# Kernel optimization log

Measured on AMD Instinct MI355X. Metric: run time of the kernel, lower is better.

Reference implementation:

```python
import jax, jax.numpy as jnp
import numpy as np
import math

N_HEAD = 32
HEAD_DIM = 64
ROTARY_DIM = 32
ROTARY_BASE = 10000.0
NEG_INF = -10000.0


def _rope_cos_sin(seqlen):
    # RotaryEmbedding._update_cos_sin_cache: inv_freq over even indices of rotary_dim
    inv_freq = 1.0 / (ROTARY_BASE ** (jnp.arange(0, ROTARY_DIM, 2, dtype=jnp.float32) / ROTARY_DIM))
    t = jnp.arange(seqlen, dtype=jnp.float32)
    freqs = jnp.outer(t, inv_freq)  # [s, rd/2]
    return jnp.cos(freqs), jnp.sin(freqs)


def _apply_rotary(t, cos, sin):
    # t: [b, s, h, d]; GPT-NeoX half-rotation on first ROTARY_DIM dims, pass-through rest
    half = ROTARY_DIM // 2
    x1 = t[..., :half]
    x2 = t[..., half:ROTARY_DIM]
    x_pass = t[..., ROTARY_DIM:]
    c = cos[:, None, :]  # [s, 1, rd/2] -> broadcasts over (b, s, h, rd/2)
    s_ = sin[:, None, :]
    return jnp.concatenate([x1 * c - x2 * s_, x1 * s_ + x2 * c, x_pass], axis=-1)


def setup_inputs() -> dict:
    key = jax.random.key(0)
    k1, k2, k3, k4, k5 = jax.random.split(key, 5)
    b, s, e = 2, 2048, 2048
    return {
        "x": jax.random.normal(k1, (b, s, e), dtype=jnp.float32),
        "Wqkv": jax.random.normal(k2, (e, 3 * e), dtype=jnp.float32) * 0.02,
        "bqkv": jax.random.normal(k3, (3 * e,), dtype=jnp.float32) * 0.02,
        "Wout": jax.random.normal(k4, (e, e), dtype=jnp.float32) * 0.02,
        "bout": jax.random.normal(k5, (e,), dtype=jnp.float32) * 0.02,
    }


def reference(x, Wqkv, bqkv, Wout, bout):
    b, s, e = x.shape
    # QKV projection -> [b, s, 3, h, d]
    qkv = (x @ Wqkv + bqkv).reshape(b, s, 3, N_HEAD, HEAD_DIM)
    cos, sin = _rope_cos_sin(s)
    q = _apply_rotary(qkv[:, :, 0], cos, sin)
    k = _apply_rotary(qkv[:, :, 1], cos, sin)
    v = qkv[:, :, 2]
    # Attention (SelfAttention/CrossAttention math, fp32, materialized scores)
    scale = 1.0 / math.sqrt(HEAD_DIM)
    scores = jnp.einsum('bthd,bshd->bhts', q, k * scale)  # [b, h, s, s]
    rows = jnp.arange(s)[:, None]
    cols = jnp.arange(s)[None, :]
    causal_mask = cols > rows  # seqlen_q == seqlen_k
    scores = jnp.where(causal_mask, NEG_INF, scores)
    attn = jax.nn.softmax(scores, axis=-1)
    out = jnp.einsum('bhts,bshd->bthd', attn, v).reshape(b, s, e)
    return out @ Wout + bout
```

## Files before the change

### kernel.cpp

```cpp
#include <hip/hip_runtime.h>


typedef _Float16 half8 __attribute__((ext_vector_type(8)));
typedef _Float16 half4 __attribute__((ext_vector_type(4)));
typedef float floatx4 __attribute__((ext_vector_type(4)));

#define GLD_LDS16(gp, sp)                                        \
  __builtin_amdgcn_global_load_lds(                              \
      (__attribute__((address_space(1))) void*)(gp),             \
      (__attribute__((address_space(3))) void*)(sp), 16, 0, 0)

__device__ __forceinline__ floatx4 mfma16(half8 a, half8 b, floatx4 c) {
  return __builtin_amdgcn_mfma_f32_16x16x32_f16(a, b, c, 0, 0, 0);
}
__device__ __forceinline__ floatx4 mfma16k16(half4 a, half4 b, floatx4 c) {
  return __builtin_amdgcn_mfma_f32_16x16x16f16(a, b, c, 0, 0, 0);
}

__global__ __launch_bounds__(256) void cvt_x_kernel(const float* __restrict__ x,
                                                    _Float16* __restrict__ xh) {
  int idx = blockIdx.x * 256 + threadIdx.x;
  const floatx4* p = (const floatx4*)x + (size_t)idx * 2;
  floatx4 a = p[0], b = p[1];
  half8 o;
#pragma unroll
  for (int j = 0; j < 4; ++j) { o[j] = (_Float16)a[j]; o[4 + j] = (_Float16)b[j]; }
  *((half8*)xh + idx) = o;
}

__global__ __launch_bounds__(256) void cvt_wt_kernel(const float* __restrict__ W,
                                                     _Float16* __restrict__ Wt,
                                                     int Kd, int Nd) {
  __shared__ float tile[64][65];
  int n0 = blockIdx.x * 64, k0 = blockIdx.y * 64;
  int tid = threadIdx.x;
#pragma unroll
  for (int it = 0; it < 4; ++it) {
    int r = (tid >> 4) + it * 16;
    int c = (tid & 15) * 4;
    floatx4 v = *(const floatx4*)(W + (size_t)(k0 + r) * Nd + n0 + c);
    tile[r][c + 0] = v[0]; tile[r][c + 1] = v[1];
    tile[r][c + 2] = v[2]; tile[r][c + 3] = v[3];
  }
  __syncthreads();
#pragma unroll
  for (int it = 0; it < 2; ++it) {
    int r = (tid >> 3) + it * 32;
    int c = (tid & 7) * 8;
    half8 o;
#pragma unroll
    for (int j = 0; j < 8; ++j) o[j] = (_Float16)tile[c + j][r];
    *(half8*)(Wt + (size_t)(n0 + r) * Kd + k0 + c) = o;
  }
}

__global__ __launch_bounds__(512, 2) void gemm256_kernel(
    const _Float16* __restrict__ A, const _Float16* __restrict__ Bt,
    const float* __restrict__ bias,
    _Float16* __restrict__ Qd, _Float16* __restrict__ Kkd,
    _Float16* __restrict__ Vd) {
  __shared__ __align__(16) _Float16 sA[2][16384];
  __shared__ __align__(16) _Float16 sB[2][16384];
  constexpr int KD = 2048;
  constexpr int NT = KD / 64;

  int tid = threadIdx.x, w = tid >> 6, l = tid & 63;
  int lr = l & 15, quad = l >> 4;
  int wr = w >> 2, wc = w & 3;
  int m0 = blockIdx.y * 256, n0 = blockIdx.x * 256;

  int csw0 = ((quad) ^ (lr & 7)) * 8;
  int csw1 = ((quad + 4) ^ (lr & 7)) * 8;

  const _Float16* pA[2][2];
  const _Float16* pB[2][2];
  {
    int Rl0 = w * 16 + (l >> 3);
    int cs = ((l & 7) ^ (l >> 3)) * 8;
#pragma unroll
    for (int h = 0; h < 2; ++h) {
#pragma unroll
      for (int j = 0; j < 2; ++j) {
        int R = Rl0 + j * 8;
        int rA = (R >> 6) * 128 + h * 64 + (R & 63);
        int rB = ((R >> 5) & 3) * 64 + h * 32 + (R & 31);
        pA[h][j] = A + (size_t)(m0 + rA) * KD + cs;
        pB[h][j] = Bt + (size_t)(n0 + rB) * KD + cs;
      }
    }
  }

#define STAGE_A(BUF, H, KT)                                                  \
  GLD_LDS16(pA[H][0] + (KT), &sA[BUF][(H) * 8192 + (w * 2 + 0) * 512]);      \
  GLD_LDS16(pA[H][1] + (KT), &sA[BUF][(H) * 8192 + (w * 2 + 1) * 512]);
#define STAGE_B(BUF, H, KT)                                                  \
  GLD_LDS16(pB[H][0] + (KT), &sB[BUF][(H) * 8192 + (w * 2 + 0) * 512]);      \
  GLD_LDS16(pB[H][1] + (KT), &sB[BUF][(H) * 8192 + (w * 2 + 1) * 512]);

#define LDA(BUF, MH)                                                         \
  _Pragma("unroll") for (int i = 0; i < 4; ++i) {                            \
    int row_ = (MH) * 128 + wr * 64 + i * 16 + lr;                           \
    af[i][0] = *(const half8*)&sA[BUF][row_ * 64 + csw0];                    \
    af[i][1] = *(const half8*)&sA[BUF][row_ * 64 + csw1];                    \
  }
#define LDB(BUF, NH)                                                         \
  _Pragma("unroll") for (int j2 = 0; j2 < 2; ++j2) {                         \
    int row_ = (NH) * 128 + wc * 32 + j2 * 16 + lr;                          \
    bf[(NH) * 2 + j2][0] = *(const half8*)&sB[BUF][row_ * 64 + csw0];        \
    bf[(NH) * 2 + j2][1] = *(const half8*)&sB[BUF][row_ * 64 + csw1];        \
  }
#define DO_MFMA(MH, NH)                                                      \
  __builtin_amdgcn_s_setprio(1);                                             \
  _Pragma("unroll") for (int ks = 0; ks < 2; ++ks)                           \
  _Pragma("unroll") for (int i = 0; i < 4; ++i)                              \
  _Pragma("unroll") for (int jj = 0; jj < 2; ++jj)                           \
    acc[(MH) * 4 + i][(NH) * 2 + jj] = mfma16(                               \
        af[i][ks], bf[(NH) * 2 + jj][ks], acc[(MH) * 4 + i][(NH) * 2 + jj]); \
  __builtin_amdgcn_s_setprio(0);

  floatx4 z4 = {0.f, 0.f, 0.f, 0.f};
  floatx4 acc[8][4];
#pragma unroll
  for (int i = 0; i < 8; ++i)
#pragma unroll
    for (int j = 0; j < 4; ++j) acc[i][j] = z4;

  STAGE_A(0, 0, 0);
  STAGE_B(0, 0, 0);
  STAGE_A(0, 1, 0);
  STAGE_B(0, 1, 0);
  STAGE_A(1, 0, 64);
  STAGE_B(1, 1, 64);
  asm volatile("s_waitcnt vmcnt(4)" ::: "memory");
  __builtin_amdgcn_s_barrier();

  half8 af[4][2], bf[4][2];
#pragma unroll 2
  for (int t = 0; t < NT; ++t) {
    int buf = t & 1, nbuf = buf ^ 1;
    int kt1 = (t + 1) * 64, kt2 = (t + 2) * 64;
    LDA(buf, 0);
    LDB(buf, 0);
    if (t + 1 < NT) { STAGE_B(nbuf, 0, kt1); STAGE_A(nbuf, 1, kt1); }
    __builtin_amdgcn_s_barrier();
    DO_MFMA(0, 0);
    LDB(buf, 1);
    __builtin_amdgcn_s_barrier();
    DO_MFMA(0, 1);
    LDA(buf, 1);
    if (t + 2 < NT) { STAGE_A(buf, 0, kt2); }
    __builtin_amdgcn_s_barrier();
    DO_MFMA(1, 1);
    if (t + 2 < NT) { STAGE_B(buf, 1, kt2); }
    asm volatile("s_waitcnt vmcnt(4)" ::: "memory");
    __builtin_amdgcn_s_barrier();
    DO_MFMA(1, 0);
  }

  int which = n0 >> 11;
  float bj[4];
#pragma unroll
  for (int j = 0; j < 4; ++j) bj[j] = bias[n0 + wc * 64 + j * 16 + lr];
  int hh = ((n0 & 2047) >> 6) + wc;
  if (which == 2) {
#pragma unroll
    for (int j = 0; j < 4; ++j) {
      int dd = j * 16 + lr;
#pragma unroll
      for (int i = 0; i < 8; ++i) {
        int m = m0 + wr * 128 + i * 16 + quad * 4;
        int bb = m >> 11, tt = m & 2047;
        half4 h;
#pragma unroll
        for (int r = 0; r < 4; ++r) h[r] = (_Float16)(acc[i][j][r] + bj[j]);
        *(half4*)&Vd[(((size_t)(bb * 32 + hh)) * 64 + dd) * 2048 + tt] = h;
      }
    }
  } else {
    _Float16* dst = which ? Kkd : Qd;
    float freq = __expf(-(float)lr * 0.57564627324851148f);
#pragma unroll
    for (int i = 0; i < 8; ++i)
#pragma unroll
      for (int r = 0; r < 4; ++r) {
        int m = m0 + wr * 128 + i * 16 + quad * 4 + r;
        int bb = m >> 11, tt = m & 2047;
        float sn, cs2;
        __sincosf((float)tt * freq, &sn, &cs2);
        float x1 = acc[i][0][r] + bj[0];
        float x2 = acc[i][1][r] + bj[1];
        _Float16* row = dst + ((size_t)(bb * 32 + hh) * 2048 + (size_t)tt) * 64;
        row[lr] = (_Float16)(x1 * cs2 - x2 * sn);
        row[lr + 16] = (_Float16)(x1 * sn + x2 * cs2);
        row[lr + 32] = (_Float16)(acc[i][2][r] + bj[2]);
        row[lr + 48] = (_Float16)(acc[i][3][r] + bj[3]);
      }
  }
#undef STAGE_A
#undef STAGE_B
#undef LDA
#undef LDB
#undef DO_MFMA
}

template <int MODE>
__global__ __launch_bounds__(256) void gemm_f16_kernel(
    const _Float16* __restrict__ A, const _Float16* __restrict__ Bt,
    const float* __restrict__ bias, int Kd, int Nd,
    _Float16* __restrict__ Qd, _Float16* __restrict__ Kkd,
    _Float16* __restrict__ Vd, float* __restrict__ Co) {
  __shared__ __align__(16) _Float16 sA[128 * 64];
  __shared__ __align__(16) _Float16 sB[128 * 64];
  int tid = threadIdx.x, w = tid >> 6, l = tid & 63;
  int lr = l & 15, lq = l >> 4;
  int m0 = blockIdx.y * 128, n0 = blockIdx.x * 128;
  int wrow = (w >> 1) * 64, wcol = (w & 1) * 64;

  floatx4 z4 = {0.f, 0.f, 0.f, 0.f};
  floatx4 acc[4][4];
#pragma unroll
  for (int i = 0; i < 4; ++i)
#pragma unroll
    for (int j = 0; j < 4; ++j) acc[i][j] = z4;

  int srow = l >> 3;
  int slot = (l & 7) ^ srow;
  const _Float16* aG = A + (size_t)(m0 + w * 32 + srow) * Kd + slot * 8;
  const _Float16* bG = Bt + (size_t)(n0 + w * 32 + srow) * Kd + slot * 8;
  _Float16* sAw = &sA[w * 2048];
  _Float16* sBw = &sB[w * 2048];

  for (int kt = 0; kt < Kd; kt += 64) {
#pragma unroll
    for (int t = 0; t < 4; ++t) {
      GLD_LDS16(aG + (size_t)t * 8 * Kd + kt, sAw + t * 512);
      GLD_LDS16(bG + (size_t)t * 8 * Kd + kt, sBw + t * 512);
    }
    __syncthreads();
#pragma unroll
    for (int ks = 0; ks < 2; ++ks) {
      half8 af[4], bf[4];
#pragma unroll
      for (int i = 0; i < 4; ++i) {
        int ar = wrow + i * 16 + lr;
        int br = wcol + i * 16 + lr;
        int sl = (((ks << 2) | lq) ^ (lr & 7)) * 8;
        af[i] = *(const half8*)&sA[ar * 64 + sl];
        bf[i] = *(const half8*)&sB[br * 64 + sl];
      }
#pragma unroll
      for (int i = 0; i < 4; ++i)
#pragma unroll
        for (int j = 0; j < 4; ++j) acc[i][j] = mfma16(af[i], bf[j], acc[i][j]);
    }
    __syncthreads();
  }

  if (MODE == 0) {
    int which = n0 >> 11;
    float bj[4];
#pragma unroll
    for (int j = 0; j < 4; ++j) bj[j] = bias[n0 + wcol + j * 16 + lr];
    int hh = ((n0 & 2047) + wcol) >> 6;
    if (which == 2) {
#pragma unroll
      for (int j = 0; j < 4; ++j) {
        int dd = j * 16 + lr;
#pragma unroll
        for (int i = 0; i < 4; ++i) {
          int m = m0 + wrow + i * 16 + lq * 4;
          int bb = m >> 11, t = m & 2047;
          half4 h;
#pragma unroll
          for (int r = 0; r < 4; ++r) h[r] = (_Float16)(acc[i][j][r] + bj[j]);
          *(half4*)&Vd[(((size_t)(bb * 32 + hh)) * 64 + dd) * 2048 + t] = h;
        }
      }
    } else {
      _Float16* dst = which ? Kkd : Qd;
      float freq = __expf(-(float)lr * 0.57564627324851148f);
#pragma unroll
      for (int i = 0; i < 4; ++i)
#pragma unroll
        for (int r = 0; r < 4; ++r) {
          int m = m0 + wrow + i * 16 + lq * 4 + r;
          int bb = m >> 11, t = m & 2047;
          float sn, cs;
          __sincosf((float)t * freq, &sn, &cs);
          float x1 = acc[i][0][r] + bj[0];
          float x2 = acc[i][1][r] + bj[1];
          _Float16* row = dst + ((size_t)(bb * 32 + hh) * 2048 + (size_t)t) * 64;
          row[lr]      = (_Float16)(x1 * cs - x2 * sn);
          row[lr + 16] = (_Float16)(x1 * sn + x2 * cs);
          row[lr + 32] = (_Float16)(acc[i][2][r] + bj[2]);
          row[lr + 48] = (_Float16)(acc[i][3][r] + bj[3]);
        }
    }
  } else {
#pragma unroll
    for (int j = 0; j < 4; ++j) {
      int n = n0 + wcol + j * 16 + lr;
      float bj = bias[n];
#pragma unroll
      for (int i = 0; i < 4; ++i)
#pragma unroll
        for (int r = 0; r < 4; ++r) {
          int m = m0 + wrow + i * 16 + lq * 4 + r;
          Co[(size_t)m * Nd + n] = acc[i][j][r] + bj;
        }
    }
  }
}

__global__ __launch_bounds__(256) void attn_kernel(
    const _Float16* __restrict__ Q, const _Float16* __restrict__ Kk,
    const _Float16* __restrict__ Vt, _Float16* __restrict__ O) {
  constexpr int S = 2048;
  int bh = blockIdx.x;
  int by = blockIdx.y;
  int bb = bh >> 5, hh = bh & 31;
  const _Float16* Qb = Q + (size_t)bh * S * 64;
  const _Float16* Kb = Kk + (size_t)bh * S * 64;
  const _Float16* Vb = Vt + (size_t)bh * 64 * S;

  __shared__ __align__(16) _Float16 sK[128 * 72];
  __shared__ __align__(16) _Float16 sVt[64 * 136];

  int tid = threadIdx.x, w = tid >> 6, l = tid & 63;
  int lr = l & 15, quad = l >> 4;

  int rk = tid >> 3, ck = (tid & 7) * 8;
  int rv = tid >> 4, cv = (tid & 15) * 8;
  const _Float16* Kst = Kb + (size_t)rk * 64 + ck;
  const _Float16* Vst = Vb + (size_t)rv * S + cv;

  int qts[2] = {15 - by, by};
  floatx4 z4 = {0.f, 0.f, 0.f, 0.f};

  for (int h = 0; h < 2; ++h) {
    int qt = qts[h];
    int q0 = qt * 128;

    half8 qf[2][2];
#pragma unroll
    for (int qtl = 0; qtl < 2; ++qtl)
#pragma unroll
      for (int ks = 0; ks < 2; ++ks) {
        half8 v = *(const half8*)(Qb + (size_t)(q0 + w * 32 + qtl * 16 + lr) * 64 +
                                  ks * 32 + quad * 8);
        qf[qtl][ks] = v * (_Float16)0.18033688f;
      }

    floatx4 Oa[4][2];
    float m_i[2] = {-1e30f, -1e30f}, l_i[2] = {0.f, 0.f};
#pragma unroll
    for (int dt = 0; dt < 4; ++dt)
#pragma unroll
      for (int qtl = 0; qtl < 2; ++qtl) Oa[dt][qtl] = z4;

    half8 kpre[4], vpre[4];
#pragma unroll
    for (int it = 0; it < 4; ++it) {
      kpre[it] = *(const half8*)(Kst + (size_t)it * 32 * 64);
      vpre[it] = *(const half8*)(Vst + (size_t)it * 16 * S);
    }

    for (int jt = 0; jt <= qt; ++jt) {
#pragma unroll
      for (int it = 0; it < 4; ++it) {
        *(half8*)&sK[(rk + it * 32) * 72 + ck] = kpre[it];
        *(half8*)&sVt[(rv + it * 16) * 136 + cv] = vpre[it];
      }
      if (jt < qt) {
        int kv1 = (jt + 1) * 128;
#pragma unroll
        for (int it = 0; it < 4; ++it) {
          kpre[it] = *(const half8*)(Kst + (size_t)(kv1 + it * 32) * 64);
          vpre[it] = *(const half8*)(Vst + kv1 + (size_t)it * 16 * S);
        }
      }
      __syncthreads();

      floatx4 Sa[2][8];
#pragma unroll
      for (int qtl = 0; qtl < 2; ++qtl)
#pragma unroll
        for (int kvt = 0; kvt < 8; ++kvt) Sa[qtl][kvt] = z4;
      __builtin_amdgcn_s_setprio(1);
#pragma unroll
      for (int ks = 0; ks < 2; ++ks) {
#pragma unroll
        for (int kvt = 0; kvt < 8; ++kvt) {
          half8 kf = *(const half8*)&sK[(kvt * 16 + lr) * 72 + ks * 32 + quad * 8];
          Sa[0][kvt] = mfma16(kf, qf[0][ks], Sa[0][kvt]);
          Sa[1][kvt] = mfma16(kf, qf[1][ks], Sa[1][kvt]);
        }
      }
      __builtin_amdgcn_s_setprio(0);

      if (jt == qt) {
#pragma unroll
        for (int qtl = 0; qtl < 2; ++qtl) {
          int q_loc = w * 32 + qtl * 16 + lr;
#pragma unroll
          for (int kvt = 0; kvt < 8; ++kvt) {
            int kv_base = kvt * 16 + quad * 4;
#pragma unroll
            for (int r = 0; r < 4; ++r)
              if (kv_base + r > q_loc) Sa[qtl][kvt][r] = -1e30f;
          }
        }
      }

#pragma unroll
      for (int qtl = 0; qtl < 2; ++qtl) {
        float mx = Sa[qtl][0][0];
#pragma unroll
        for (int kvt = 0; kvt < 8; ++kvt)
#pragma unroll
          for (int r = 0; r < 4; ++r) mx = fmaxf(mx, Sa[qtl][kvt][r]);
        mx = fmaxf(mx, __shfl_xor(mx, 16));
        mx = fmaxf(mx, __shfl_xor(mx, 32));
        float mnew = fmaxf(m_i[qtl], mx);
        float alpha = __builtin_amdgcn_exp2f(m_i[qtl] - mnew);
        m_i[qtl] = mnew;
        float rs = 0.f;
#pragma unroll
        for (int kvt = 0; kvt < 8; ++kvt)
#pragma unroll
          for (int r = 0; r < 4; ++r) {
            float p = __builtin_amdgcn_exp2f(Sa[qtl][kvt][r] - mnew);
            Sa[qtl][kvt][r] = p;
            rs += p;
          }
        rs += __shfl_xor(rs, 16);
        rs += __shfl_xor(rs, 32);
        l_i[qtl] = l_i[qtl] * alpha + rs;
#pragma unroll
        for (int dt = 0; dt < 4; ++dt) Oa[dt][qtl] *= alpha;
      }

      __builtin_amdgcn_s_setprio(1);
#pragma unroll
      for (int kvt = 0; kvt < 8; ++kvt) {
        half4 vf[4];
#pragma unroll
        for (int dt = 0; dt < 4; ++dt)
          vf[dt] = *(const half4*)&sVt[(dt * 16 + lr) * 136 + kvt * 16 + quad * 4];
        half4 pf[2];
#pragma unroll
        for (int qtl = 0; qtl < 2; ++qtl) {
          pf[qtl][0] = (_Float16)Sa[qtl][kvt][0];
          pf[qtl][1] = (_Float16)Sa[qtl][kvt][1];
          pf[qtl][2] = (_Float16)Sa[qtl][kvt][2];
          pf[qtl][3] = (_Float16)Sa[qtl][kvt][3];
        }
#pragma unroll
        for (int dt = 0; dt < 4; ++dt)
#pragma unroll
          for (int qtl = 0; qtl < 2; ++qtl)
            Oa[dt][qtl] = mfma16k16(vf[dt], pf[qtl], Oa[dt][qtl]);
      }
      __builtin_amdgcn_s_setprio(0);
      __syncthreads();
    }

    float inv0 = 1.0f / l_i[0], inv1 = 1.0f / l_i[1];
#pragma unroll
    for (int dt = 0; dt < 4; ++dt)
#pragma unroll
      for (int qtl = 0; qtl < 2; ++qtl) {
        float inv = qtl ? inv1 : inv0;
        floatx4 o = Oa[dt][qtl];
        half4 hv;
        hv[0] = (_Float16)(o[0] * inv); hv[1] = (_Float16)(o[1] * inv);
        hv[2] = (_Float16)(o[2] * inv); hv[3] = (_Float16)(o[3] * inv);
        *(half4*)&sK[(w * 32 + qtl * 16 + lr) * 72 + dt * 16 + quad * 4] = hv;
      }
    __syncthreads();
#pragma unroll
    for (int it = 0; it < 2; ++it) {
      int row = (tid >> 2) + it * 64;
      int t = q0 + row;
      _Float16* orow = O + ((size_t)(bb * 2048 + t)) * 2048 + hh * 64;
#pragma unroll
      for (int cc = 0; cc < 2; ++cc) {
        int col = (tid & 3) * 16 + cc * 8;
        *(half8*)(orow + col) = *(const half8*)&sK[row * 72 + col];
      }
    }
    __syncthreads();
  }
}

extern "C" void kernel_launch(void* const* d_in, const int* in_sizes, int n_in,
                              void* d_out, int out_size, void* d_ws, size_t ws_size,
                              hipStream_t stream) {
  (void)in_sizes; (void)n_in; (void)out_size; (void)ws_size;
  const float* x = (const float*)d_in[0];
  const float* Wqkv = (const float*)d_in[1];
  const float* bqkv = (const float*)d_in[2];
  const float* Wout = (const float*)d_in[3];
  const float* bout = (const float*)d_in[4];
  float* out = (float*)d_out;
  char* ws = (char*)d_ws;

  _Float16* xh    = (_Float16*)(ws + 0);
  _Float16* wqkvt = (_Float16*)(ws + 16777216);
  _Float16* Oh    = (_Float16*)(ws + 16777216);
  _Float16* Qh    = (_Float16*)(ws + 41943040);
  _Float16* Kh    = (_Float16*)(ws + 58720256);
  _Float16* Vth   = (_Float16*)(ws + 75497472);
  _Float16* woutt = (_Float16*)(ws + 92274688);

  cvt_x_kernel<<<4096, 256, 0, stream>>>(x, xh);
  cvt_wt_kernel<<<dim3(96, 32), 256, 0, stream>>>(Wqkv, wqkvt, 2048, 6144);
  cvt_wt_kernel<<<dim3(32, 32), 256, 0, stream>>>(Wout, woutt, 2048, 2048);
  gemm256_kernel<<<dim3(24, 16), 512, 0, stream>>>(xh, wqkvt, bqkv, Qh, Kh, Vth);
  attn_kernel<<<dim3(64, 8), 256, 0, stream>>>(Qh, Kh, Vth, Oh);
  gemm_f16_kernel<1><<<dim3(16, 32), 256, 0, stream>>>(
      Oh, woutt, bout, 2048, 2048, nullptr, nullptr, nullptr, out);
}
```

Baseline: 394.4 us.

## Reschedule QKV GEMM main loop into quarter phases with double-buffered A fragments

```diff
diff --git a/kernel.cpp b/kernel.cpp
--- a/kernel.cpp
+++ b/kernel.cpp
@@ -97,25 +97,24 @@
   GLD_LDS16(pB[H][0] + (KT), &sB[BUF][(H) * 8192 + (w * 2 + 0) * 512]);      \
   GLD_LDS16(pB[H][1] + (KT), &sB[BUF][(H) * 8192 + (w * 2 + 1) * 512]);
 
-#define LDA(BUF, MH)                                                         \
-  _Pragma("unroll") for (int i = 0; i < 4; ++i) {                            \
-    int row_ = (MH) * 128 + wr * 64 + i * 16 + lr;                           \
-    af[i][0] = *(const half8*)&sA[BUF][row_ * 64 + csw0];                    \
-    af[i][1] = *(const half8*)&sA[BUF][row_ * 64 + csw1];                    \
-  }
-#define LDB(BUF, NH)                                                         \
+#define LDAP(AF, BUF, P)                                                     \
+  _Pragma("unroll") for (int i = 0; i < 2; ++i) {                            \
+    int row_ = ((P) >> 1) * 128 + wr * 64 + (((P) & 1) * 2 + i) * 16 + lr;   \
+    AF[i][0] = *(const half8*)&sA[BUF][row_ * 64 + csw0];                    \
+    AF[i][1] = *(const half8*)&sA[BUF][row_ * 64 + csw1];                    \
+  }
+#define LDBH(NH, BUF)                                                        \
   _Pragma("unroll") for (int j2 = 0; j2 < 2; ++j2) {                         \
     int row_ = (NH) * 128 + wc * 32 + j2 * 16 + lr;                          \
     bf[(NH) * 2 + j2][0] = *(const half8*)&sB[BUF][row_ * 64 + csw0];        \
     bf[(NH) * 2 + j2][1] = *(const half8*)&sB[BUF][row_ * 64 + csw1];        \
   }
-#define DO_MFMA(MH, NH)                                                      \
+#define MFMA_P(P, AF)                                                        \
   __builtin_amdgcn_s_setprio(1);                                             \
+  _Pragma("unroll") for (int j = 0; j < 4; ++j)                              \
   _Pragma("unroll") for (int ks = 0; ks < 2; ++ks)                           \
-  _Pragma("unroll") for (int i = 0; i < 4; ++i)                              \
-  _Pragma("unroll") for (int jj = 0; jj < 2; ++jj)                           \
-    acc[(MH) * 4 + i][(NH) * 2 + jj] = mfma16(                               \
-        af[i][ks], bf[(NH) * 2 + jj][ks], acc[(MH) * 4 + i][(NH) * 2 + jj]); \
+  _Pragma("unroll") for (int i = 0; i < 2; ++i)                              \
+    acc[2 * (P) + i][j] = mfma16(AF[i][ks], bf[j][ks], acc[2 * (P) + i][j]); \
   __builtin_amdgcn_s_setprio(0);
 
   floatx4 z4 = {0.f, 0.f, 0.f, 0.f};
@@ -134,27 +133,37 @@
   asm volatile("s_waitcnt vmcnt(4)" ::: "memory");
   __builtin_amdgcn_s_barrier();
 
-  half8 af[4][2], bf[4][2];
+  half8 afA[2][2], afB[2][2], bf[4][2];
+  LDAP(afA, 0, 0);
+  LDBH(0, 0);
+
 #pragma unroll 2
   for (int t = 0; t < NT; ++t) {
     int buf = t & 1, nbuf = buf ^ 1;
     int kt1 = (t + 1) * 64, kt2 = (t + 2) * 64;
-    LDA(buf, 0);
-    LDB(buf, 0);
-    if (t + 1 < NT) { STAGE_B(nbuf, 0, kt1); STAGE_A(nbuf, 1, kt1); }
+    LDAP(afB, buf, 1);
+    LDBH(1, buf);
+    if (t + 1 < NT) { STAGE_B(nbuf, 0, kt1); }
     __builtin_amdgcn_s_barrier();
-    DO_MFMA(0, 0);
-    LDB(buf, 1);
+    MFMA_P(0, afA);
+    LDAP(afA, buf, 2);
+    if (t + 1 < NT) { STAGE_A(nbuf, 1, kt1); }
     __builtin_amdgcn_s_barrier();
-    DO_MFMA(0, 1);
-    LDA(buf, 1);
+    MFMA_P(1, afB);
+    LDAP(afB, buf, 3);
     if (t + 2 < NT) { STAGE_A(buf, 0, kt2); }
     __builtin_amdgcn_s_barrier();
-    DO_MFMA(1, 1);
-    if (t + 2 < NT) { STAGE_B(buf, 1, kt2); }
-    asm volatile("s_waitcnt vmcnt(4)" ::: "memory");
+    MFMA_P(2, afA);
+    if (t + 2 < NT) {
+      STAGE_B(buf, 1, kt2);
+      asm volatile("s_waitcnt vmcnt(4)" ::: "memory");
+    } else {
+      asm volatile("s_waitcnt vmcnt(0)" ::: "memory");
+    }
     __builtin_amdgcn_s_barrier();
-    DO_MFMA(1, 0);
+    if (t + 1 < NT) { LDAP(afA, nbuf, 0); }
+    MFMA_P(3, afB);
+    if (t + 1 < NT) { LDBH(0, nbuf); }
   }
 
   int which = n0 >> 11;
@@ -198,9 +207,9 @@
   }
 #undef STAGE_A
 #undef STAGE_B
-#undef LDA
-#undef LDB
-#undef DO_MFMA
+#undef LDAP
+#undef LDBH
+#undef MFMA_P
 }
 
 template <int MODE>
```

After: 399.4 us. About the same (+1.3%).

## Restructure QKV GEMM pipeline to prefetch two full k-tiles ahead

Applied to the files above, without the earlier changes.

```diff
diff --git a/kernel.cpp b/kernel.cpp
--- a/kernel.cpp
+++ b/kernel.cpp
@@ -109,7 +109,7 @@
     bf[(NH) * 2 + j2][0] = *(const half8*)&sB[BUF][row_ * 64 + csw0];        \
     bf[(NH) * 2 + j2][1] = *(const half8*)&sB[BUF][row_ * 64 + csw1];        \
   }
-#define DO_MFMA(MH, NH)                                                      \
+#define MFMA_Q(MH, NH)                                                       \
   __builtin_amdgcn_s_setprio(1);                                             \
   _Pragma("unroll") for (int ks = 0; ks < 2; ++ks)                           \
   _Pragma("unroll") for (int i = 0; i < 4; ++i)                              \
@@ -127,34 +127,44 @@
 
   STAGE_A(0, 0, 0);
   STAGE_B(0, 0, 0);
+  STAGE_B(0, 1, 0);
   STAGE_A(0, 1, 0);
-  STAGE_B(0, 1, 0);
   STAGE_A(1, 0, 64);
+  STAGE_B(1, 0, 64);
   STAGE_B(1, 1, 64);
-  asm volatile("s_waitcnt vmcnt(4)" ::: "memory");
+  STAGE_A(1, 1, 64);
+  asm volatile("s_waitcnt vmcnt(8)" ::: "memory");
   __builtin_amdgcn_s_barrier();
 
   half8 af[4][2], bf[4][2];
 #pragma unroll 2
   for (int t = 0; t < NT; ++t) {
-    int buf = t & 1, nbuf = buf ^ 1;
-    int kt1 = (t + 1) * 64, kt2 = (t + 2) * 64;
+    int buf = t & 1;
+    int kt2 = (t + 2) * 64;
     LDA(buf, 0);
     LDB(buf, 0);
-    if (t + 1 < NT) { STAGE_B(nbuf, 0, kt1); STAGE_A(nbuf, 1, kt1); }
-    __builtin_amdgcn_s_barrier();
-    DO_MFMA(0, 0);
+    __builtin_amdgcn_s_barrier();
+    MFMA_Q(0, 0);
+    __builtin_amdgcn_s_barrier();
     LDB(buf, 1);
-    __builtin_amdgcn_s_barrier();
-    DO_MFMA(0, 1);
+    if (t + 2 < NT) { STAGE_A(buf, 0, kt2); STAGE_B(buf, 0, kt2); }
+    __builtin_amdgcn_s_barrier();
+    MFMA_Q(0, 1);
+    __builtin_amdgcn_s_barrier();
     LDA(buf, 1);
-    if (t + 2 < NT) { STAGE_A(buf, 0, kt2); }
-    __builtin_amdgcn_s_barrier();
-    DO_MFMA(1, 1);
     if (t + 2 < NT) { STAGE_B(buf, 1, kt2); }
-    asm volatile("s_waitcnt vmcnt(4)" ::: "memory");
-    __builtin_amdgcn_s_barrier();
-    DO_MFMA(1, 0);
+    __builtin_amdgcn_s_barrier();
+    MFMA_Q(1, 1);
+    __builtin_amdgcn_s_barrier();
+    if (t + 2 < NT) {
+      STAGE_A(buf, 1, kt2);
+      asm volatile("s_waitcnt vmcnt(8)" ::: "memory");
+    } else {
+      asm volatile("s_waitcnt vmcnt(0)" ::: "memory");
+    }
+    __builtin_amdgcn_s_barrier();
+    MFMA_Q(1, 0);
+    __builtin_amdgcn_s_barrier();
   }
 
   int which = n0 >> 11;
@@ -200,7 +210,7 @@
 #undef STAGE_B
 #undef LDA
 #undef LDB
-#undef DO_MFMA
+#undef MFMA_Q
 }
 
 template <int MODE>
```

New measurement: 399.8 us. About the same (+1.4%).
